# Optimization experiments

Hardware: AMD Instinct MI355X
Metric: run time of the kernel (lower is better)

Reference implementation:

```python
import jax, jax.numpy as jnp
import numpy as np

ALG_DIM = 248      # dim of E8 adjoint rep
NNZ_BASE = 300     # base structure-constant triples (antisymmetrized -> 600 nnz)
N_NODES = 20000
N_EDGES = 160000


def _structure_constants():
    """Deterministic sparse antisymmetric structure constants C_ijk.

    Returns index arrays (ci, cj, ck) int32 and values cv float32 such that
    [x, y]_k = sum_t cv[t] * x[ci[t]] * y[cj[t]] with C antisymmetric in (i, j).
    """
    rng = np.random.default_rng(0)
    i = rng.integers(0, ALG_DIM, NNZ_BASE)
    j = rng.integers(0, ALG_DIM, NNZ_BASE)
    j = np.where(j == i, (j + 1) % ALG_DIM, j)  # bracket of equal basis elts is 0
    k = rng.integers(0, ALG_DIM, NNZ_BASE)
    v = rng.normal(size=NNZ_BASE).astype(np.float32)
    ci = np.concatenate([i, j]).astype(np.int32)
    cj = np.concatenate([j, i]).astype(np.int32)
    ck = np.concatenate([k, k]).astype(np.int32)
    cv = np.concatenate([v, -v]).astype(np.float32)
    return jnp.asarray(ci), jnp.asarray(cj), jnp.asarray(ck), jnp.asarray(cv)


def _bracket(x, y, ci, cj, ck, cv):
    """Sparse Lie bracket [x, y]: x, y have shape (..., ALG_DIM)."""
    terms = x[..., ci] * y[..., cj] * cv          # (..., nnz)
    return jnp.zeros(x.shape, x.dtype).at[..., ck].add(terms)


def setup_inputs() -> dict:
    key = jax.random.key(0)
    k1, k2 = jax.random.split(key)
    features = jax.random.normal(k1, (N_NODES, ALG_DIM), dtype=jnp.float32)
    edge_index = jax.random.randint(k2, (2, N_EDGES), 0, N_NODES, dtype=jnp.int32)
    ci, cj, ck, cv = _structure_constants()
    return {
        "features": features,
        "edge_index": edge_index,
        "ci": ci, "cj": cj, "ck": ck, "cv": cv,
        "alpha_msg": jnp.float32(1.0),     # msg_projection.alpha
        "alpha_bil": jnp.float32(1.0),     # msg_bilinear.alpha
        "alpha_w": jnp.float32(1.0),       # update_W.alpha
        "update_scale": jnp.float32(0.1),
    }


def reference(features, edge_index, ci, cj, ck, cv,
              alpha_msg, alpha_bil, alpha_w, update_scale):
    src_idx = edge_index[0]
    tgt_idx = edge_index[1]
    src = features[src_idx]                        # (E, d) gather
    tgt = features[tgt_idx]                        # (E, d) gather
    # message: alpha_bil * [alpha_msg * src, tgt]
    msg = alpha_bil * _bracket(alpha_msg * src, tgt, ci, cj, ck, cv)
    # scatter-add aggregate into per-node accumulator
    agg = jnp.zeros_like(features).at[tgt_idx].add(msg)
    # bracket-based update: x + agg + scale * [agg, alpha_w * agg]
    upd = _bracket(agg, alpha_w * agg, ci, cj, ck, cv)
    return features + agg + update_scale * upd
```

## Files before the change

kernel.cpp:

```cpp
#include <hip/hip_runtime.h>


#define ALG    248
#define ALG4    62
#define SLOTS   64
#define WPB      4
#define NBLK  2500
#define MAXSL    8

struct __align__(8) Term { unsigned int ijk; float v; };

__global__ __launch_bounds__(256) void elc_fill(
    const int* __restrict__ ei, int E,
    int* __restrict__ cnt, int* __restrict__ slot)
{
    for (int e = blockIdx.x * 256 + threadIdx.x; e < E; e += gridDim.x * 256) {
        const int t = ei[E + e];
        const int p = atomicAdd(&cnt[t], 1);
        if (p < SLOTS) slot[t * SLOTS + p] = ei[e];
    }
}

__global__ __launch_bounds__(256, 4) void elc_node(
    const float* __restrict__ feat,
    const int*   __restrict__ cnt,
    const int*   __restrict__ slot,
    const int*   __restrict__ ci, const int* __restrict__ cj,
    const int*   __restrict__ ck, const float* __restrict__ cv,
    const float* __restrict__ p_am, const float* __restrict__ p_ab,
    float* __restrict__ out, int N, int nnz)
{
    __shared__ Term s_terms[MAXSL * 64];
    __shared__ __align__(16) float s_buf[WPB][512];
    __shared__ __align__(16) float s_ag[WPB][256];

    const int tid  = threadIdx.x;
    const int lane = tid & 63;
    const int wave = tid >> 6;

    const int nnzB = nnz >> 1;
    int nSl = (nnzB + 63) >> 6;
    if (nSl > MAXSL) nSl = MAXSL;

    {
        const int nT = nSl << 6;
        for (int t = tid; t < nT; t += 256) {
            Term tm; tm.ijk = 0u; tm.v = 0.f;
            if (t < nnzB) {
                tm.ijk = (unsigned)ci[t] | ((unsigned)cj[t] << 8)
                       | ((unsigned)ck[t] << 16);
                tm.v = cv[t];
            }
            s_terms[t] = tm;
        }
    }
    __syncthreads();

    const float cab = (*p_ab) * (*p_am);
    const float4* feat4 = (const float4*)feat;
    float* sbuf = s_buf[wave];
    float* ag   = s_ag[wave];

    auto bracket_store = [&](int nodeId, float4 Sv, float4 Tv) {
        if (lane < ALG4) {
            ((float4*)sbuf)[2 * lane]     = make_float4(Sv.x, Tv.x, Sv.y, Tv.y);
            ((float4*)sbuf)[2 * lane + 1] = make_float4(Sv.z, Tv.z, Sv.w, Tv.w);
        }
        ((float4*)ag)[lane] = make_float4(0.f, 0.f, 0.f, 0.f);

        auto doSlot = [&](int sl) {
            const Term tm = s_terms[(sl << 6) + lane];
            const int i2 = (int)((tm.ijk & 255u) << 1);
            const int j2 = (int)(((tm.ijk >> 8) & 255u) << 1);
            const float2 a = *(const float2*)(sbuf + i2);
            const float2 b = *(const float2*)(sbuf + j2);
            float d = a.x * b.y;
            d = fmaf(-b.x, a.y, d);
            atomicAdd(ag + (int)((tm.ijk >> 16) & 255u), tm.v * d);
        };
        if (nSl == 5) {
#pragma unroll
            for (int sl = 0; sl < 5; ++sl) doSlot(sl);
        } else {
            for (int sl = 0; sl < nSl; ++sl) doSlot(sl);
        }

        if (lane < ALG4) {
            const float4 av = ((const float4*)ag)[lane];
            float4 o;
            o.x = fmaf(cab, av.x, Tv.x);
            o.y = fmaf(cab, av.y, Tv.y);
            o.z = fmaf(cab, av.z, Tv.z);
            o.w = fmaf(cab, av.w, Tv.w);
            ((float4*)(out + (size_t)nodeId * ALG))[lane] = o;
        }
    };

    const int wstride = gridDim.x * WPB;
    int n = blockIdx.x * WPB + wave;

    int deg_c = 0, sn_c = 0;
    float4 tgt_c = make_float4(0.f, 0.f, 0.f, 0.f);
    if (n < N) {
        deg_c = min(cnt[n], SLOTS);
        sn_c  = slot[n * SLOTS + lane];
        if (lane < ALG4) tgt_c = feat4[(size_t)n * ALG4 + lane];
    }

    int    nP   = -1;
    float4 accP = make_float4(0.f, 0.f, 0.f, 0.f);
    float4 tgtP = make_float4(0.f, 0.f, 0.f, 0.f);

    while (n < N) {
        const int n_next = n + wstride;

        float4 f[8];
#pragma unroll
        for (int d = 0; d < 8; ++d) {
            f[d] = make_float4(0.f, 0.f, 0.f, 0.f);
            const int sd = __shfl(sn_c, d);
            if (d < deg_c && lane < ALG4)
                f[d] = feat4[(size_t)sd * ALG4 + lane];
        }

        int deg_n = 0, sn_n = 0;
        float4 tgt_n = make_float4(0.f, 0.f, 0.f, 0.f);
        if (n_next < N) {
            deg_n = min(cnt[n_next], SLOTS);
            sn_n  = slot[n_next * SLOTS + lane];
            if (lane < ALG4) tgt_n = feat4[(size_t)n_next * ALG4 + lane];
        }

        if (nP >= 0) bracket_store(nP, accP, tgtP);

        float4 acc = make_float4(0.f, 0.f, 0.f, 0.f);
#pragma unroll
        for (int d = 0; d < 8; ++d) {
            acc.x += f[d].x; acc.y += f[d].y;
            acc.z += f[d].z; acc.w += f[d].w;
        }
        for (int d = 8; d < deg_c; ++d) {
            const int sd = __shfl(sn_c, d);
            if (lane < ALG4) {
                const float4 fd = feat4[(size_t)sd * ALG4 + lane];
                acc.x += fd.x; acc.y += fd.y; acc.z += fd.z; acc.w += fd.w;
            }
        }

        nP = n; accP = acc; tgtP = tgt_c;
        n = n_next; deg_c = deg_n; sn_c = sn_n; tgt_c = tgt_n;
    }

    if (nP >= 0) bracket_store(nP, accP, tgtP);
}

extern "C" void kernel_launch(void* const* d_in, const int* in_sizes, int n_in,
                              void* d_out, int out_size, void* d_ws, size_t ws_size,
                              hipStream_t stream) {
    const float* feat = (const float*)d_in[0];
    const int*   ei   = (const int*)d_in[1];
    const int*   ci   = (const int*)d_in[2];
    const int*   cj   = (const int*)d_in[3];
    const int*   ck   = (const int*)d_in[4];
    const float* cv   = (const float*)d_in[5];
    const float* p_am = (const float*)d_in[6];
    const float* p_ab = (const float*)d_in[7];
    float* out = (float*)d_out;

    const int N   = in_sizes[0] / ALG;
    const int E   = in_sizes[1] / 2;
    const int nnz = in_sizes[5];

    char* w = (char*)d_ws;
    int* cnt  = (int*)w;                 w += (size_t)N * sizeof(int);
    int* slot = (int*)w;

    hipMemsetAsync(cnt, 0, (size_t)N * sizeof(int), stream);
    elc_fill<<<640, 256, 0, stream>>>(ei, E, cnt, slot);
    elc_node<<<NBLK, 256, 0, stream>>>(feat, cnt, slot, ci, cj, ck, cv,
                                       p_am, p_ab, out, N, nnz);
}
```

Baseline: 144.9 us.

## Process one node per wave with register-held structure constants instead of persistent loop

Replaces the persistent grid-stride loop, which prefetched the next node while bracketing the previous one, with a launch of one node per wave in 128-thread blocks. Structure-constant terms are loaded into per-lane registers instead of shared memory, removing a block barrier. Twelve neighbour rows are gathered up front before accumulation. The aim is more latency hiding through many resident waves, at the cost of losing the explicit cross-node prefetch and reloading the constants in every wave.

```diff
diff --git a/kernel.cpp b/kernel.cpp
--- a/kernel.cpp
+++ b/kernel.cpp
@@ -4,11 +4,9 @@
 #define ALG    248
 #define ALG4    62
 #define SLOTS   64
-#define WPB      4
-#define NBLK  2500
+#define WPB      2
+#define TPB    128
 #define MAXSL    8
-
-struct __align__(8) Term { unsigned int ijk; float v; };
 
 __global__ __launch_bounds__(256) void elc_fill(
     const int* __restrict__ ei, int E,
@@ -21,7 +19,7 @@
     }
 }
 
-__global__ __launch_bounds__(256, 4) void elc_node(
+__global__ __launch_bounds__(TPB, 5) void elc_node(
     const float* __restrict__ feat,
     const int*   __restrict__ cnt,
     const int*   __restrict__ slot,
@@ -30,7 +28,6 @@
     const float* __restrict__ p_am, const float* __restrict__ p_ab,
     float* __restrict__ out, int N, int nnz)
 {
-    __shared__ Term s_terms[MAXSL * 64];
     __shared__ __align__(16) float s_buf[WPB][512];
     __shared__ __align__(16) float s_ag[WPB][256];
 
@@ -42,116 +39,99 @@
     int nSl = (nnzB + 63) >> 6;
     if (nSl > MAXSL) nSl = MAXSL;
 
-    {
-        const int nT = nSl << 6;
-        for (int t = tid; t < nT; t += 256) {
-            Term tm; tm.ijk = 0u; tm.v = 0.f;
-            if (t < nnzB) {
-                tm.ijk = (unsigned)ci[t] | ((unsigned)cj[t] << 8)
-                       | ((unsigned)ck[t] << 16);
-                tm.v = cv[t];
-            }
-            s_terms[t] = tm;
+    unsigned tijk[MAXSL];
+    float    tval[MAXSL];
+#pragma unroll
+    for (int sl = 0; sl < MAXSL; ++sl) { tijk[sl] = 0u; tval[sl] = 0.f; }
+    for (int sl = 0; sl < nSl; ++sl) {
+        const int t = (sl << 6) + lane;
+        if (t < nnzB) {
+            tijk[sl] = (unsigned)ci[t] | ((unsigned)cj[t] << 8)
+                     | ((unsigned)ck[t] << 16);
+            tval[sl] = cv[t];
         }
     }
-    __syncthreads();
+
+    const int n = blockIdx.x * WPB + wave;
+    if (n >= N) return;
 
     const float cab = (*p_ab) * (*p_am);
     const float4* feat4 = (const float4*)feat;
+
+    const int deg = min(cnt[n], SLOTS);
+    const int sn  = slot[n * SLOTS + lane];
+    float4 tgt = make_float4(0.f, 0.f, 0.f, 0.f);
+    if (lane < ALG4) tgt = feat4[(size_t)n * ALG4 + lane];
+
+    float4 f[8];
+#pragma unroll
+    for (int d = 0; d < 8; ++d) {
+        f[d] = make_float4(0.f, 0.f, 0.f, 0.f);
+        const int sd = __shfl(sn, d);
+        if (d < deg && lane < ALG4)
+            f[d] = feat4[(size_t)sd * ALG4 + lane];
+    }
+    float4 g[4];
+#pragma unroll
+    for (int d = 0; d < 4; ++d) {
+        g[d] = make_float4(0.f, 0.f, 0.f, 0.f);
+        const int sd = __shfl(sn, d + 8);
+        if (d + 8 < deg && lane < ALG4)
+            g[d] = feat4[(size_t)sd * ALG4 + lane];
+    }
+
+    float4 acc = make_float4(0.f, 0.f, 0.f, 0.f);
+#pragma unroll
+    for (int d = 0; d < 8; ++d) {
+        acc.x += f[d].x; acc.y += f[d].y; acc.z += f[d].z; acc.w += f[d].w;
+    }
+#pragma unroll
+    for (int d = 0; d < 4; ++d) {
+        acc.x += g[d].x; acc.y += g[d].y; acc.z += g[d].z; acc.w += g[d].w;
+    }
+    for (int d = 12; d < deg; ++d) {
+        const int sd = __shfl(sn, d);
+        if (lane < ALG4) {
+            const float4 fd = feat4[(size_t)sd * ALG4 + lane];
+            acc.x += fd.x; acc.y += fd.y; acc.z += fd.z; acc.w += fd.w;
+        }
+    }
+
     float* sbuf = s_buf[wave];
     float* ag   = s_ag[wave];
 
-    auto bracket_store = [&](int nodeId, float4 Sv, float4 Tv) {
-        if (lane < ALG4) {
-            ((float4*)sbuf)[2 * lane]     = make_float4(Sv.x, Tv.x, Sv.y, Tv.y);
-            ((float4*)sbuf)[2 * lane + 1] = make_float4(Sv.z, Tv.z, Sv.w, Tv.w);
-        }
-        ((float4*)ag)[lane] = make_float4(0.f, 0.f, 0.f, 0.f);
+    if (lane < ALG4) {
+        ((float4*)sbuf)[2 * lane]     = make_float4(acc.x, tgt.x, acc.y, tgt.y);
+        ((float4*)sbuf)[2 * lane + 1] = make_float4(acc.z, tgt.z, acc.w, tgt.w);
+    }
+    ((float4*)ag)[lane] = make_float4(0.f, 0.f, 0.f, 0.f);
 
-        auto doSlot = [&](int sl) {
-            const Term tm = s_terms[(sl << 6) + lane];
-            const int i2 = (int)((tm.ijk & 255u) << 1);
-            const int j2 = (int)(((tm.ijk >> 8) & 255u) << 1);
-            const float2 a = *(const float2*)(sbuf + i2);
-            const float2 b = *(const float2*)(sbuf + j2);
-            float d = a.x * b.y;
-            d = fmaf(-b.x, a.y, d);
-            atomicAdd(ag + (int)((tm.ijk >> 16) & 255u), tm.v * d);
-        };
-        if (nSl == 5) {
+    auto doSlot = [&](int sl) {
+        const unsigned p = tijk[sl];
+        const int i2 = (int)((p & 255u) << 1);
+        const int j2 = (int)(((p >> 8) & 255u) << 1);
+        const float2 a = *(const float2*)(sbuf + i2);
+        const float2 b = *(const float2*)(sbuf + j2);
+        float d = a.x * b.y;
+        d = fmaf(-b.x, a.y, d);
+        atomicAdd(ag + (int)((p >> 16) & 255u), tval[sl] * d);
+    };
+    if (nSl == 5) {
 #pragma unroll
-            for (int sl = 0; sl < 5; ++sl) doSlot(sl);
-        } else {
-            for (int sl = 0; sl < nSl; ++sl) doSlot(sl);
-        }
-
-        if (lane < ALG4) {
-            const float4 av = ((const float4*)ag)[lane];
-            float4 o;
-            o.x = fmaf(cab, av.x, Tv.x);
-            o.y = fmaf(cab, av.y, Tv.y);
-            o.z = fmaf(cab, av.z, Tv.z);
-            o.w = fmaf(cab, av.w, Tv.w);
-            ((float4*)(out + (size_t)nodeId * ALG))[lane] = o;
-        }
-    };
-
-    const int wstride = gridDim.x * WPB;
-    int n = blockIdx.x * WPB + wave;
-
-    int deg_c = 0, sn_c = 0;
-    float4 tgt_c = make_float4(0.f, 0.f, 0.f, 0.f);
-    if (n < N) {
-        deg_c = min(cnt[n], SLOTS);
-        sn_c  = slot[n * SLOTS + lane];
-        if (lane < ALG4) tgt_c = feat4[(size_t)n * ALG4 + lane];
+        for (int sl = 0; sl < 5; ++sl) doSlot(sl);
+    } else {
+        for (int sl = 0; sl < nSl; ++sl) doSlot(sl);
     }
 
-    int    nP   = -1;
-    float4 accP = make_float4(0.f, 0.f, 0.f, 0.f);
-    float4 tgtP = make_float4(0.f, 0.f, 0.f, 0.f);
-
-    while (n < N) {
-        const int n_next = n + wstride;
-
-        float4 f[8];
-#pragma unroll
-        for (int d = 0; d < 8; ++d) {
-            f[d] = make_float4(0.f, 0.f, 0.f, 0.f);
-            const int sd = __shfl(sn_c, d);
-            if (d < deg_c && lane < ALG4)
-                f[d] = feat4[(size_t)sd * ALG4 + lane];
-        }
-
-        int deg_n = 0, sn_n = 0;
-        float4 tgt_n = make_float4(0.f, 0.f, 0.f, 0.f);
-        if (n_next < N) {
-            deg_n = min(cnt[n_next], SLOTS);
-            sn_n  = slot[n_next * SLOTS + lane];
-            if (lane < ALG4) tgt_n = feat4[(size_t)n_next * ALG4 + lane];
-        }
-
-        if (nP >= 0) bracket_store(nP, accP, tgtP);
-
-        float4 acc = make_float4(0.f, 0.f, 0.f, 0.f);
-#pragma unroll
-        for (int d = 0; d < 8; ++d) {
-            acc.x += f[d].x; acc.y += f[d].y;
-            acc.z += f[d].z; acc.w += f[d].w;
-        }
-        for (int d = 8; d < deg_c; ++d) {
-            const int sd = __shfl(sn_c, d);
-            if (lane < ALG4) {
-                const float4 fd = feat4[(size_t)sd * ALG4 + lane];
-                acc.x += fd.x; acc.y += fd.y; acc.z += fd.z; acc.w += fd.w;
-            }
-        }
-
-        nP = n; accP = acc; tgtP = tgt_c;
-        n = n_next; deg_c = deg_n; sn_c = sn_n; tgt_c = tgt_n;
+    if (lane < ALG4) {
+        const float4 av = ((const float4*)ag)[lane];
+        float4 o;
+        o.x = fmaf(cab, av.x, tgt.x);
+        o.y = fmaf(cab, av.y, tgt.y);
+        o.z = fmaf(cab, av.z, tgt.z);
+        o.w = fmaf(cab, av.w, tgt.w);
+        ((float4*)(out + (size_t)n * ALG))[lane] = o;
     }
-
-    if (nP >= 0) bracket_store(nP, accP, tgtP);
 }
 
 extern "C" void kernel_launch(void* const* d_in, const int* in_sizes, int n_in,
@@ -177,6 +157,8 @@
 
     hipMemsetAsync(cnt, 0, (size_t)N * sizeof(int), stream);
     elc_fill<<<640, 256, 0, stream>>>(ei, E, cnt, slot);
-    elc_node<<<NBLK, 256, 0, stream>>>(feat, cnt, slot, ci, cj, ck, cv,
+
+    const int nblk = (N + WPB - 1) / WPB;
+    elc_node<<<nblk, TPB, 0, stream>>>(feat, cnt, slot, ci, cj, ck, cv,
                                        p_am, p_ab, out, N, nnz);
 }
```

New measurement: 142.5 us. No clear change (-1.6%).
